# Kernel tuning notes

Hardware: AMD Instinct MI355X
Metric: run time of the kernel (lower is better)

The kernel has to match this reference:

```python
import jax, jax.numpy as jnp
import numpy as np

COMMITMENT_COST = 0.25  # pg_nn.VectorQuantizer default


def setup_inputs() -> dict:
    key = jax.random.key(0)
    k1, k2, k3, k4 = jax.random.split(key, 4)
    B, C, H, W = 32, 128, 64, 64
    D, K = 64, 512
    x = jax.random.normal(k1, (B, C, H, W), jnp.float32)
    # 1x1 conv == per-pixel linear projection; store weight as [D, C]
    conv_w = jax.random.normal(k2, (D, C), jnp.float32) * (1.0 / np.sqrt(C))
    conv_b = jax.random.normal(k3, (D,), jnp.float32) * 0.01
    # VectorQuantizer init: uniform(-1/K, 1/K)
    codebook = jax.random.uniform(k4, (K, D), jnp.float32, -1.0 / K, 1.0 / K)
    return {"x": x, "conv_w": conv_w, "conv_b": conv_b, "codebook": codebook}


def reference(x, conv_w, conv_b, codebook):
    # 1x1 conv projection: [B,C,H,W] -> [B,D,H,W]
    z = jnp.einsum('bchw,dc->bdhw', x, conv_w) + conv_b[None, :, None, None]
    B, D, H, W = z.shape
    flat = z.transpose(0, 2, 3, 1).reshape(-1, D)  # [B*H*W, D]
    # squared L2 distances to each codebook vector: [B*H*W, K]
    dists = (jnp.sum(flat * flat, axis=1, keepdims=True)
             - 2.0 * flat @ codebook.T
             + jnp.sum(codebook * codebook, axis=1))
    idx = jnp.argmin(dists, axis=1)  # [B*H*W]
    quantized = codebook[idx].reshape(B, H, W, D).transpose(0, 3, 1, 2)
    # VQ losses (commitment + embedding)
    commitment = COMMITMENT_COST * jnp.mean(jnp.square(jax.lax.stop_gradient(quantized) - z))
    emb_loss = jnp.mean(jnp.square(quantized - jax.lax.stop_gradient(z)))
    loss = commitment + emb_loss
    # straight-through estimator
    quantized_st = z + jax.lax.stop_gradient(quantized - z)
    return quantized_st, loss
```

## Files before the change

kernel.cpp:

```cpp
#include <hip/hip_runtime.h>
#include <hip/hip_bf16.h>
#include <math.h>

#define CIN   128
#define DDIM  64
#define KCB   512
#define HWSZ  4096
#define NOUTQ 8388608
#define XPAD  136

typedef short bf16x8 __attribute__((ext_vector_type(8)));
typedef float f32x4  __attribute__((ext_vector_type(4)));
typedef unsigned int u32x2 __attribute__((ext_vector_type(2)));

#define BLOB_B   84992
#define NCHUNK_B 83
#define WS_PART  86016

__device__ __forceinline__ unsigned int bcu(float f){ union{float f;unsigned int u;}v; v.f=f; return v.u; }
__device__ __forceinline__ float bcf(unsigned int u){ union{unsigned int u;float f;}v; v.u=u; return v.f; }
__device__ __forceinline__ unsigned int pkbf(float a, float b){
    union { __hip_bfloat162 h; unsigned int u; } v;
    v.h = __float22bfloat162_rn(make_float2(a, b));
    return v.u;
}

#define MFMA16(A, B, C) __builtin_amdgcn_mfma_f32_16x16x32_bf16((A), (B), (C), 0, 0, 0)

__global__ __launch_bounds__(256) void vq_prep(
    const float* __restrict__ cb, const float* __restrict__ w,
    const float* __restrict__ bias, unsigned char* __restrict__ blob)
{
    unsigned short* cbA = (unsigned short*)blob;
    unsigned short* wA  = (unsigned short*)(blob + 65536);
    float*          cbn = (float*)(blob + 81920);
    float*          bia = (float*)(blob + 83968);

    const int gid = blockIdx.x * 256 + threadIdx.x;
    {
        int k = gid >> 4, dg = gid & 15;
        f32x4 v = *(const f32x4*)(cb + (size_t)k * DDIM + dg * 4);
        u32x2 pv = { pkbf(-2.f * v[0], -2.f * v[1]), pkbf(-2.f * v[2], -2.f * v[3]) };
        int ct = k >> 4, ks = dg >> 3, lhi = (dg >> 1) & 3, ll = (k & 15) | (lhi << 4);
        *(u32x2*)(cbA + ((ct * 2 + ks) * 64 + ll) * 8 + (dg & 1) * 4) = pv;
    }
    if (gid < 2048) {
        int d = gid >> 5, cg = gid & 31;
        f32x4 v = *(const f32x4*)(w + (size_t)d * CIN + cg * 4);
        u32x2 pv = { pkbf(v[0], v[1]), pkbf(v[2], v[3]) };
        int dt = d >> 4, ks = cg >> 3, lhi = (cg >> 1) & 3, ll = (d & 15) | (lhi << 4);
        *(u32x2*)(wA + ((dt * 4 + ks) * 64 + ll) * 8 + (cg & 1) * 4) = pv;
    }
    if (gid < KCB) {
        const f32x4* row = (const f32x4*)(cb + (size_t)gid * DDIM);
        float s = 0.f;
        #pragma unroll
        for (int j = 0; j < DDIM / 4; ++j) {
            f32x4 v = row[j];
            s = fmaf(v[0], v[0], s); s = fmaf(v[1], v[1], s);
            s = fmaf(v[2], v[2], s); s = fmaf(v[3], v[3], s);
        }
        cbn[gid] = s;
    }
    if (gid < DDIM) bia[gid] = bias[gid];
}

__device__ __forceinline__ void proj_tile(
    const float (&xr)[32], unsigned short* xrow,
    const unsigned short* sWA, const float* sBias,
    int lg, int klg, int l,
    f32x4& zA, f32x4& zB, f32x4& zC, f32x4& zD, bf16x8& zb0, bf16x8& zb1)
{
    #pragma unroll
    for (int j = 0; j < 8; ++j) {
        u32x2 pv = { pkbf(xr[4*j+0], xr[4*j+1]), pkbf(xr[4*j+2], xr[4*j+3]) };
        *(u32x2*)(xrow + lg * 32 + 4 * j) = pv;
    }
    zA = *(const f32x4*)(sBias +  0 + klg);
    zB = *(const f32x4*)(sBias + 16 + klg);
    zC = *(const f32x4*)(sBias + 32 + klg);
    zD = *(const f32x4*)(sBias + 48 + klg);
    #pragma unroll
    for (int ks = 0; ks < 4; ++ks) {
        bf16x8 xf = *(const bf16x8*)(xrow + ks * 32 + lg * 8);
        bf16x8 w0 = *(const bf16x8*)(sWA + ((0 * 4 + ks) * 64 + l) * 8);
        bf16x8 w1 = *(const bf16x8*)(sWA + ((1 * 4 + ks) * 64 + l) * 8);
        bf16x8 w2 = *(const bf16x8*)(sWA + ((2 * 4 + ks) * 64 + l) * 8);
        bf16x8 w3 = *(const bf16x8*)(sWA + ((3 * 4 + ks) * 64 + l) * 8);
        zA = MFMA16(w0, xf, zA);
        zB = MFMA16(w1, xf, zB);
        zC = MFMA16(w2, xf, zC);
        zD = MFMA16(w3, xf, zD);
    }
    unsigned int* zr = (unsigned int*)xrow;
    u32x2 z0 = { pkbf(zA[0], zA[1]), pkbf(zA[2], zA[3]) };
    u32x2 z1 = { pkbf(zB[0], zB[1]), pkbf(zB[2], zB[3]) };
    u32x2 z2 = { pkbf(zC[0], zC[1]), pkbf(zC[2], zC[3]) };
    u32x2 z3 = { pkbf(zD[0], zD[1]), pkbf(zD[2], zD[3]) };
    *(u32x2*)(zr +  0 + lg * 2) = z0;
    *(u32x2*)(zr +  8 + lg * 2) = z1;
    *(u32x2*)(zr + 16 + lg * 2) = z2;
    *(u32x2*)(zr + 24 + lg * 2) = z3;
    zb0 = *(const bf16x8*)(xrow + lg * 8);
    zb1 = *(const bf16x8*)(xrow + 32 + lg * 8);
}

__global__ __launch_bounds__(1024, 4) void vq_mfma(
    const float* __restrict__ x,
    const float* __restrict__ cb,
    const unsigned char* __restrict__ blob,
    float* __restrict__ out,
    float* __restrict__ part)
{
    __shared__ __align__(16) unsigned char sFrag[BLOB_B];
    __shared__ __align__(16) unsigned short sX[16 * 16 * XPAD];
    __shared__ float sLoss[16];

    const int t   = threadIdx.x;
    const int l   = t & 63;
    const int wv  = t >> 6;
    const int p16 = l & 15;
    const int lg  = l >> 4;
    const int klg = lg * 4;

    for (int i = wv; i < NCHUNK_B; i += 16) {
        const unsigned char* g = blob + i * 1024 + l * 16;
        unsigned char* s = sFrag + i * 1024;
        __builtin_amdgcn_global_load_lds(
            (const __attribute__((address_space(1))) unsigned int*)g,
            (__attribute__((address_space(3))) unsigned int*)s, 16, 0, 0);
    }

    const int b   = blockIdx.x >> 3;
    const int hw0 = (blockIdx.x & 7) * 512 + wv * 32;
    const float* xp = x + ((size_t)b * CIN + (size_t)lg * 32) * HWSZ + hw0 + p16;
    float xr0[32], xr1[32];
    #pragma unroll
    for (int j = 0; j < 32; ++j) {
        xr0[j] = xp[(size_t)j * HWSZ];
        xr1[j] = xp[(size_t)j * HWSZ + 16];
    }
    __syncthreads();

    const unsigned short* sCbA = (const unsigned short*)sFrag;
    const unsigned short* sWA  = (const unsigned short*)(sFrag + 65536);
    const float*          sCbn = (const float*)(sFrag + 81920);
    const float*          sBias= (const float*)(sFrag + 83968);

    unsigned short* xrow = sX + wv * (16 * XPAD) + p16 * XPAD;

    f32x4 zaA0, zaA1, zaA2, zaA3, zaB0, zaB1, zaB2, zaB3;
    bf16x8 zb00, zb01, zb10, zb11;
    proj_tile(xr0, xrow, sWA, sBias, lg, klg, l, zaA0, zaA1, zaA2, zaA3, zb00, zb01);
    proj_tile(xr1, xrow, sWA, sBias, lg, klg, l, zaB0, zaB1, zaB2, zaB3, zb10, zb11);

    float rm00 = INFINITY, rm01 = INFINITY, rm10 = INFINITY, rm11 = INFINITY;
    #pragma unroll 4
    for (int ct = 0; ct < 32; ++ct) {
        f32x4 cinit = *(const f32x4*)(sCbn + ct * 16 + klg);
        bf16x8 c0 = *(const bf16x8*)(sCbA + ((ct * 2 + 0) * 64 + l) * 8);
        bf16x8 c1 = *(const bf16x8*)(sCbA + ((ct * 2 + 1) * 64 + l) * 8);
        f32x4 a0 = MFMA16(c0, zb00, cinit); a0 = MFMA16(c1, zb01, a0);
        f32x4 a1 = MFMA16(c0, zb10, cinit); a1 = MFMA16(c1, zb11, a1);
        unsigned int kb = (unsigned int)(ct * 16 + klg);
        rm00 = fminf(rm00, bcf((bcu(a0[0]) & 0xFFFFFE00u) | (kb + 0)));
        rm01 = fminf(rm01, bcf((bcu(a0[1]) & 0xFFFFFE00u) | (kb + 1)));
        rm00 = fminf(rm00, bcf((bcu(a0[2]) & 0xFFFFFE00u) | (kb + 2)));
        rm01 = fminf(rm01, bcf((bcu(a0[3]) & 0xFFFFFE00u) | (kb + 3)));
        rm10 = fminf(rm10, bcf((bcu(a1[0]) & 0xFFFFFE00u) | (kb + 0)));
        rm11 = fminf(rm11, bcf((bcu(a1[1]) & 0xFFFFFE00u) | (kb + 1)));
        rm10 = fminf(rm10, bcf((bcu(a1[2]) & 0xFFFFFE00u) | (kb + 2)));
        rm11 = fminf(rm11, bcf((bcu(a1[3]) & 0xFFFFFE00u) | (kb + 3)));
    }
    float rn0 = fminf(rm00, rm01);
    rn0 = fminf(rn0, __shfl_xor(rn0, 16, 64));
    rn0 = fminf(rn0, __shfl_xor(rn0, 32, 64));
    const int kbest0 = (int)(bcu(rn0) & 511u);
    float rn1 = fminf(rm10, rm11);
    rn1 = fminf(rn1, __shfl_xor(rn1, 16, 64));
    rn1 = fminf(rn1, __shfl_xor(rn1, 32, 64));
    const int kbest1 = (int)(bcu(rn1) & 511u);

    const float* q0r = cb + (size_t)kbest0 * DDIM;
    const float* q1r = cb + (size_t)kbest1 * DDIM;
    f32x4 qa0 = *(const f32x4*)(q0r +  0 + klg), qb0 = *(const f32x4*)(q1r +  0 + klg);
    f32x4 qa1 = *(const f32x4*)(q0r + 16 + klg), qb1 = *(const f32x4*)(q1r + 16 + klg);
    f32x4 qa2 = *(const f32x4*)(q0r + 32 + klg), qb2 = *(const f32x4*)(q1r + 32 + klg);
    f32x4 qa3 = *(const f32x4*)(q0r + 48 + klg), qb3 = *(const f32x4*)(q1r + 48 + klg);
    float lsum = 0.f;
    size_t ob = ((size_t)b * DDIM + klg) * (size_t)HWSZ + hw0 + p16;
    #pragma unroll
    for (int r = 0; r < 4; ++r) {
        float e;
        e = qa0[r] - zaA0[r]; lsum = fmaf(e, e, lsum);
        e = qb0[r] - zaB0[r]; lsum = fmaf(e, e, lsum);
        e = qa1[r] - zaA1[r]; lsum = fmaf(e, e, lsum);
        e = qb1[r] - zaB1[r]; lsum = fmaf(e, e, lsum);
        e = qa2[r] - zaA2[r]; lsum = fmaf(e, e, lsum);
        e = qb2[r] - zaB2[r]; lsum = fmaf(e, e, lsum);
        e = qa3[r] - zaA3[r]; lsum = fmaf(e, e, lsum);
        e = qb3[r] - zaB3[r]; lsum = fmaf(e, e, lsum);
        out[ob + (size_t)(r +  0) * HWSZ]      = qa0[r];
        out[ob + (size_t)(r +  0) * HWSZ + 16] = qb0[r];
        out[ob + (size_t)(r + 16) * HWSZ]      = qa1[r];
        out[ob + (size_t)(r + 16) * HWSZ + 16] = qb1[r];
        out[ob + (size_t)(r + 32) * HWSZ]      = qa2[r];
        out[ob + (size_t)(r + 32) * HWSZ + 16] = qb2[r];
        out[ob + (size_t)(r + 48) * HWSZ]      = qa3[r];
        out[ob + (size_t)(r + 48) * HWSZ + 16] = qb3[r];
    }

    #pragma unroll
    for (int off = 32; off > 0; off >>= 1)
        lsum += __shfl_down(lsum, off, 64);
    if (l == 0) sLoss[wv] = lsum;
    __syncthreads();
    if (wv == 0) {
        float v = (l < 16) ? sLoss[l] : 0.f;
        v += __shfl_down(v, 8, 64);
        v += __shfl_down(v, 4, 64);
        v += __shfl_down(v, 2, 64);
        v += __shfl_down(v, 1, 64);
        if (l == 0) part[blockIdx.x] = v;
    }
}

__global__ __launch_bounds__(256) void vq_loss(
    const float* __restrict__ part, float* __restrict__ loss_slot)
{
    __shared__ float sW[4];
    const int t = threadIdx.x;
    float s = part[t];
    #pragma unroll
    for (int off = 32; off > 0; off >>= 1) s += __shfl_down(s, off, 64);
    if ((t & 63) == 0) sW[t >> 6] = s;
    __syncthreads();
    if (t == 0)
        *loss_slot = (sW[0] + sW[1] + sW[2] + sW[3]) * (1.25f / (float)NOUTQ);
}

extern "C" void kernel_launch(void* const* d_in, const int* in_sizes, int n_in,
                              void* d_out, int out_size, void* d_ws, size_t ws_size,
                              hipStream_t stream) {
    const float* x    = (const float*)d_in[0];
    const float* w    = (const float*)d_in[1];
    const float* bias = (const float*)d_in[2];
    const float* cb   = (const float*)d_in[3];
    float* out = (float*)d_out;
    float* loss_slot = out + NOUTQ;

    unsigned char* blob = (unsigned char*)d_ws;
    float* part = (float*)(blob + WS_PART);

    vq_prep<<<32,  256,  0, stream>>>(cb, w, bias, blob);
    vq_mfma<<<256, 1024, 0, stream>>>(x, cb, blob, out, part);
    vq_loss<<<1,   256,  0, stream>>>(part, loss_slot);
}
```

Measured before the change: 42.56 us.

## Fuse loss reduction via last-block ticket and overlap x loads with LDS blob copy

Removes the separate loss-reduction kernel: each block writes its partial, increments an atomic ticket, and the last block sums all partials and writes the loss. The __syncthreads after the loads is replaced by a partial vmcnt wait plus a raw s_barrier, so the x register loads can stay in flight while the LDS blob copy completes. Launch bounds are relaxed from 4 to 2 waves per EU, which allows more registers. The partial vmcnt(48) relies on the hardware retiring memory operations in issue order, and the ticket scheme depends on a threadfence and relaxed atomic loads to be correct.

```diff
diff --git a/kernel.cpp b/kernel.cpp
--- a/kernel.cpp
+++ b/kernel.cpp
@@ -16,6 +16,7 @@
 #define BLOB_B   84992
 #define NCHUNK_B 83
 #define WS_PART  86016
+#define WS_TICK  87040
 
 __device__ __forceinline__ unsigned int bcu(float f){ union{float f;unsigned int u;}v; v.f=f; return v.u; }
 __device__ __forceinline__ float bcf(unsigned int u){ union{unsigned int u;float f;}v; v.u=u; return v.f; }
@@ -29,7 +30,8 @@
 
 __global__ __launch_bounds__(256) void vq_prep(
     const float* __restrict__ cb, const float* __restrict__ w,
-    const float* __restrict__ bias, unsigned char* __restrict__ blob)
+    const float* __restrict__ bias, unsigned char* __restrict__ blob,
+    unsigned int* __restrict__ ticket)
 {
     unsigned short* cbA = (unsigned short*)blob;
     unsigned short* wA  = (unsigned short*)(blob + 65536);
@@ -63,6 +65,7 @@
         cbn[gid] = s;
     }
     if (gid < DDIM) bia[gid] = bias[gid];
+    if (gid == 0) *ticket = 0u;
 }
 
 __device__ __forceinline__ void proj_tile(
@@ -105,12 +108,13 @@
     zb1 = *(const bf16x8*)(xrow + 32 + lg * 8);
 }
 
-__global__ __launch_bounds__(1024, 4) void vq_mfma(
+__global__ __launch_bounds__(1024, 2) void vq_mfma(
     const float* __restrict__ x,
     const float* __restrict__ cb,
     const unsigned char* __restrict__ blob,
     float* __restrict__ out,
-    float* __restrict__ part)
+    float* __restrict__ part,
+    unsigned int* __restrict__ ticket)
 {
     __shared__ __align__(16) unsigned char sFrag[BLOB_B];
     __shared__ __align__(16) unsigned short sX[16 * 16 * XPAD];
@@ -130,6 +134,7 @@
             (const __attribute__((address_space(1))) unsigned int*)g,
             (__attribute__((address_space(3))) unsigned int*)s, 16, 0, 0);
     }
+    __builtin_amdgcn_sched_barrier(0);
 
     const int b   = blockIdx.x >> 3;
     const int hw0 = (blockIdx.x & 7) * 512 + wv * 32;
@@ -140,7 +145,10 @@
         xr0[j] = xp[(size_t)j * HWSZ];
         xr1[j] = xp[(size_t)j * HWSZ + 16];
     }
-    __syncthreads();
+    __builtin_amdgcn_sched_barrier(0);
+    asm volatile("s_waitcnt vmcnt(48)" ::: "memory");
+    __builtin_amdgcn_s_barrier();
+    __builtin_amdgcn_sched_barrier(0);
 
     const unsigned short* sCbA = (const unsigned short*)sFrag;
     const unsigned short* sWA  = (const unsigned short*)(sFrag + 65536);
@@ -221,22 +229,25 @@
         v += __shfl_down(v, 4, 64);
         v += __shfl_down(v, 2, 64);
         v += __shfl_down(v, 1, 64);
-        if (l == 0) part[blockIdx.x] = v;
-    }
-}
-
-__global__ __launch_bounds__(256) void vq_loss(
-    const float* __restrict__ part, float* __restrict__ loss_slot)
-{
-    __shared__ float sW[4];
-    const int t = threadIdx.x;
-    float s = part[t];
-    #pragma unroll
-    for (int off = 32; off > 0; off >>= 1) s += __shfl_down(s, off, 64);
-    if ((t & 63) == 0) sW[t >> 6] = s;
-    __syncthreads();
-    if (t == 0)
-        *loss_slot = (sW[0] + sW[1] + sW[2] + sW[3]) * (1.25f / (float)NOUTQ);
+        unsigned int old = 0u;
+        if (l == 0) {
+            part[blockIdx.x] = v;
+            __threadfence();
+            old = atomicAdd(ticket, 1u);
+        }
+        old = __shfl((int)old, 0, 64);
+        if (old == 255u) {
+            float s = 0.f;
+            #pragma unroll
+            for (int j = 0; j < 4; ++j)
+                s += __hip_atomic_load(&part[l + j * 64],
+                                       __ATOMIC_RELAXED, __HIP_MEMORY_SCOPE_AGENT);
+            #pragma unroll
+            for (int off = 32; off > 0; off >>= 1)
+                s += __shfl_down(s, off, 64);
+            if (l == 0) out[NOUTQ] = s * (1.25f / (float)NOUTQ);
+        }
+    }
 }
 
 extern "C" void kernel_launch(void* const* d_in, const int* in_sizes, int n_in,
@@ -247,12 +258,11 @@
     const float* bias = (const float*)d_in[2];
     const float* cb   = (const float*)d_in[3];
     float* out = (float*)d_out;
-    float* loss_slot = out + NOUTQ;
 
     unsigned char* blob = (unsigned char*)d_ws;
     float* part = (float*)(blob + WS_PART);
-
-    vq_prep<<<32,  256,  0, stream>>>(cb, w, bias, blob);
-    vq_mfma<<<256, 1024, 0, stream>>>(x, cb, blob, out, part);
-    vq_loss<<<1,   256,  0, stream>>>(part, loss_slot);
-}
+    unsigned int* tick = (unsigned int*)(blob + WS_TICK);
+
+    vq_prep<<<32,  256,  0, stream>>>(cb, w, bias, blob, tick);
+    vq_mfma<<<256, 1024, 0, stream>>>(x, cb, blob, out, part, tick);
+}
```

Result: slower. 51.53 us (+21.1%).

## Load x straight into bf16 MFMA fragments and derive loss from min distances

Applied to the files above, without the earlier changes.

Each lane now reads and packs x directly into bf16 MFMA operand fragments, so the per-wave LDS staging of x and its round trip are gone and the LDS buffer shrinks to a z-only tile. The VQ loss is now computed algebraically as the selected minimum distance plus ||z||^2, which removes the per-element (q - z)^2 work. The quantized output is written with a new mapping where each lane stores 32 channels for one pixel, making stores coalesced across pixels. The risk is loss precision: the minimum distance comes from bf16 MFMA with index bits packed into the mantissa.

```diff
diff --git a/kernel.cpp b/kernel.cpp
--- a/kernel.cpp
+++ b/kernel.cpp
@@ -7,7 +7,7 @@
 #define KCB   512
 #define HWSZ  4096
 #define NOUTQ 8388608
-#define XPAD  136
+#define ZPAD  72
 
 typedef short bf16x8 __attribute__((ext_vector_type(8)));
 typedef float f32x4  __attribute__((ext_vector_type(4)));
@@ -65,34 +65,45 @@
     if (gid < DDIM) bia[gid] = bias[gid];
 }
 
-__device__ __forceinline__ void proj_tile(
-    const float (&xr)[32], unsigned short* xrow,
-    const unsigned short* sWA, const float* sBias,
+#define LOADXF(xq, lgv, F0, F1, F2, F3)                                     \
+    {                                                                       \
+        union { unsigned int u[4]; bf16x8 v; } c0_, c1_, c2_, c3_;          \
+        _Pragma("unroll")                                                   \
+        for (int p = 0; p < 4; ++p) {                                       \
+            const float* a0 = (xq) + (size_t)(  0 + (lgv)*8 + 2*p) * HWSZ;  \
+            const float* a1 = (xq) + (size_t)( 32 + (lgv)*8 + 2*p) * HWSZ;  \
+            const float* a2 = (xq) + (size_t)( 64 + (lgv)*8 + 2*p) * HWSZ;  \
+            const float* a3 = (xq) + (size_t)( 96 + (lgv)*8 + 2*p) * HWSZ;  \
+            c0_.u[p] = pkbf(a0[0], a0[HWSZ]);                               \
+            c1_.u[p] = pkbf(a1[0], a1[HWSZ]);                               \
+            c2_.u[p] = pkbf(a2[0], a2[HWSZ]);                               \
+            c3_.u[p] = pkbf(a3[0], a3[HWSZ]);                               \
+        }                                                                   \
+        F0 = c0_.v; F1 = c1_.v; F2 = c2_.v; F3 = c3_.v;                     \
+    }
+
+__device__ __forceinline__ void proj_mfma(
+    bf16x8 f0, bf16x8 f1, bf16x8 f2, bf16x8 f3,
+    unsigned short* zrow, const unsigned short* sWA, const float* sBias,
     int lg, int klg, int l,
     f32x4& zA, f32x4& zB, f32x4& zC, f32x4& zD, bf16x8& zb0, bf16x8& zb1)
 {
-    #pragma unroll
-    for (int j = 0; j < 8; ++j) {
-        u32x2 pv = { pkbf(xr[4*j+0], xr[4*j+1]), pkbf(xr[4*j+2], xr[4*j+3]) };
-        *(u32x2*)(xrow + lg * 32 + 4 * j) = pv;
-    }
     zA = *(const f32x4*)(sBias +  0 + klg);
     zB = *(const f32x4*)(sBias + 16 + klg);
     zC = *(const f32x4*)(sBias + 32 + klg);
     zD = *(const f32x4*)(sBias + 48 + klg);
-    #pragma unroll
-    for (int ks = 0; ks < 4; ++ks) {
-        bf16x8 xf = *(const bf16x8*)(xrow + ks * 32 + lg * 8);
-        bf16x8 w0 = *(const bf16x8*)(sWA + ((0 * 4 + ks) * 64 + l) * 8);
-        bf16x8 w1 = *(const bf16x8*)(sWA + ((1 * 4 + ks) * 64 + l) * 8);
-        bf16x8 w2 = *(const bf16x8*)(sWA + ((2 * 4 + ks) * 64 + l) * 8);
-        bf16x8 w3 = *(const bf16x8*)(sWA + ((3 * 4 + ks) * 64 + l) * 8);
-        zA = MFMA16(w0, xf, zA);
-        zB = MFMA16(w1, xf, zB);
-        zC = MFMA16(w2, xf, zC);
-        zD = MFMA16(w3, xf, zD);
-    }
-    unsigned int* zr = (unsigned int*)xrow;
+    #define PSTEP(ks, xf) {                                             \
+        bf16x8 w0 = *(const bf16x8*)(sWA + ((0 * 4 + ks) * 64 + l) * 8);\
+        bf16x8 w1 = *(const bf16x8*)(sWA + ((1 * 4 + ks) * 64 + l) * 8);\
+        bf16x8 w2 = *(const bf16x8*)(sWA + ((2 * 4 + ks) * 64 + l) * 8);\
+        bf16x8 w3 = *(const bf16x8*)(sWA + ((3 * 4 + ks) * 64 + l) * 8);\
+        zA = MFMA16(w0, xf, zA);                                        \
+        zB = MFMA16(w1, xf, zB);                                        \
+        zC = MFMA16(w2, xf, zC);                                        \
+        zD = MFMA16(w3, xf, zD); }
+    PSTEP(0, f0) PSTEP(1, f1) PSTEP(2, f2) PSTEP(3, f3)
+    #undef PSTEP
+    unsigned int* zr = (unsigned int*)zrow;
     u32x2 z0 = { pkbf(zA[0], zA[1]), pkbf(zA[2], zA[3]) };
     u32x2 z1 = { pkbf(zB[0], zB[1]), pkbf(zB[2], zB[3]) };
     u32x2 z2 = { pkbf(zC[0], zC[1]), pkbf(zC[2], zC[3]) };
@@ -101,8 +112,8 @@
     *(u32x2*)(zr +  8 + lg * 2) = z1;
     *(u32x2*)(zr + 16 + lg * 2) = z2;
     *(u32x2*)(zr + 24 + lg * 2) = z3;
-    zb0 = *(const bf16x8*)(xrow + lg * 8);
-    zb1 = *(const bf16x8*)(xrow + 32 + lg * 8);
+    zb0 = *(const bf16x8*)(zrow + lg * 8);
+    zb1 = *(const bf16x8*)(zrow + 32 + lg * 8);
 }
 
 __global__ __launch_bounds__(1024, 4) void vq_mfma(
@@ -113,7 +124,7 @@
     float* __restrict__ part)
 {
     __shared__ __align__(16) unsigned char sFrag[BLOB_B];
-    __shared__ __align__(16) unsigned short sX[16 * 16 * XPAD];
+    __shared__ __align__(16) unsigned short sZ[16 * 16 * ZPAD];
     __shared__ float sLoss[16];
 
     const int t   = threadIdx.x;
@@ -133,26 +144,24 @@
 
     const int b   = blockIdx.x >> 3;
     const int hw0 = (blockIdx.x & 7) * 512 + wv * 32;
-    const float* xp = x + ((size_t)b * CIN + (size_t)lg * 32) * HWSZ + hw0 + p16;
-    float xr0[32], xr1[32];
-    #pragma unroll
-    for (int j = 0; j < 32; ++j) {
-        xr0[j] = xp[(size_t)j * HWSZ];
-        xr1[j] = xp[(size_t)j * HWSZ + 16];
-    }
+    const float* xq = x + (size_t)b * CIN * HWSZ + hw0 + p16;
+    bf16x8 xa0, xa1, xa2, xa3, xb0, xb1, xb2, xb3;
+    LOADXF(xq,      lg, xa0, xa1, xa2, xa3)
+    LOADXF(xq + 16, lg, xb0, xb1, xb2, xb3)
     __syncthreads();
 
     const unsigned short* sCbA = (const unsigned short*)sFrag;
     const unsigned short* sWA  = (const unsigned short*)(sFrag + 65536);
     const float*          sCbn = (const float*)(sFrag + 81920);
     const float*          sBias= (const float*)(sFrag + 83968);
-
-    unsigned short* xrow = sX + wv * (16 * XPAD) + p16 * XPAD;
+    unsigned short* zrow = sZ + wv * (16 * ZPAD) + p16 * ZPAD;
 
     f32x4 zaA0, zaA1, zaA2, zaA3, zaB0, zaB1, zaB2, zaB3;
     bf16x8 zb00, zb01, zb10, zb11;
-    proj_tile(xr0, xrow, sWA, sBias, lg, klg, l, zaA0, zaA1, zaA2, zaA3, zb00, zb01);
-    proj_tile(xr1, xrow, sWA, sBias, lg, klg, l, zaB0, zaB1, zaB2, zaB3, zb10, zb11);
+    proj_mfma(xa0, xa1, xa2, xa3, zrow, sWA, sBias, lg, klg, l,
+              zaA0, zaA1, zaA2, zaA3, zb00, zb01);
+    proj_mfma(xb0, xb1, xb2, xb3, zrow, sWA, sBias, lg, klg, l,
+              zaB0, zaB1, zaB2, zaB3, zb10, zb11);
 
     float rm00 = INFINITY, rm01 = INFINITY, rm10 = INFINITY, rm11 = INFINITY;
     #pragma unroll 4
@@ -181,39 +190,40 @@
     rn1 = fminf(rn1, __shfl_xor(rn1, 32, 64));
     const int kbest1 = (int)(bcu(rn1) & 511u);
 
-    const float* q0r = cb + (size_t)kbest0 * DDIM;
-    const float* q1r = cb + (size_t)kbest1 * DDIM;
-    f32x4 qa0 = *(const f32x4*)(q0r +  0 + klg), qb0 = *(const f32x4*)(q1r +  0 + klg);
-    f32x4 qa1 = *(const f32x4*)(q0r + 16 + klg), qb1 = *(const f32x4*)(q1r + 16 + klg);
-    f32x4 qa2 = *(const f32x4*)(q0r + 32 + klg), qb2 = *(const f32x4*)(q1r + 32 + klg);
-    f32x4 qa3 = *(const f32x4*)(q0r + 48 + klg), qb3 = *(const f32x4*)(q1r + 48 + klg);
-    float lsum = 0.f;
-    size_t ob = ((size_t)b * DDIM + klg) * (size_t)HWSZ + hw0 + p16;
+    float zn0 = 0.f, zn1 = 0.f;
     #pragma unroll
     for (int r = 0; r < 4; ++r) {
-        float e;
-        e = qa0[r] - zaA0[r]; lsum = fmaf(e, e, lsum);
-        e = qb0[r] - zaB0[r]; lsum = fmaf(e, e, lsum);
-        e = qa1[r] - zaA1[r]; lsum = fmaf(e, e, lsum);
-        e = qb1[r] - zaB1[r]; lsum = fmaf(e, e, lsum);
-        e = qa2[r] - zaA2[r]; lsum = fmaf(e, e, lsum);
-        e = qb2[r] - zaB2[r]; lsum = fmaf(e, e, lsum);
-        e = qa3[r] - zaA3[r]; lsum = fmaf(e, e, lsum);
-        e = qb3[r] - zaB3[r]; lsum = fmaf(e, e, lsum);
-        out[ob + (size_t)(r +  0) * HWSZ]      = qa0[r];
-        out[ob + (size_t)(r +  0) * HWSZ + 16] = qb0[r];
-        out[ob + (size_t)(r + 16) * HWSZ]      = qa1[r];
-        out[ob + (size_t)(r + 16) * HWSZ + 16] = qb1[r];
-        out[ob + (size_t)(r + 32) * HWSZ]      = qa2[r];
-        out[ob + (size_t)(r + 32) * HWSZ + 16] = qb2[r];
-        out[ob + (size_t)(r + 48) * HWSZ]      = qa3[r];
-        out[ob + (size_t)(r + 48) * HWSZ + 16] = qb3[r];
-    }
-
+        zn0 = fmaf(zaA0[r], zaA0[r], zn0); zn0 = fmaf(zaA1[r], zaA1[r], zn0);
+        zn0 = fmaf(zaA2[r], zaA2[r], zn0); zn0 = fmaf(zaA3[r], zaA3[r], zn0);
+        zn1 = fmaf(zaB0[r], zaB0[r], zn1); zn1 = fmaf(zaB1[r], zaB1[r], zn1);
+        zn1 = fmaf(zaB2[r], zaB2[r], zn1); zn1 = fmaf(zaB3[r], zaB3[r], zn1);
+    }
+    zn0 += __shfl_xor(zn0, 16, 64); zn0 += __shfl_xor(zn0, 32, 64);
+    zn1 += __shfl_xor(zn1, 16, 64); zn1 += __shfl_xor(zn1, 32, 64);
+
+    {
+        const int px = l & 31;
+        const int dh = (l >> 5) * 32;
+        const int kbs = (px & 16) ? kbest1 : kbest0;
+        const f32x4* qv = (const f32x4*)(cb + (size_t)kbs * DDIM + dh);
+        f32x4 q0 = qv[0], q1 = qv[1], q2 = qv[2], q3 = qv[3];
+        f32x4 q4 = qv[4], q5 = qv[5], q6 = qv[6], q7 = qv[7];
+        size_t base = ((size_t)b * DDIM + dh) * (size_t)HWSZ + hw0 + px;
+        #define QST(i, qq) \
+            out[base + (size_t)(4*(i)+0) * HWSZ] = qq[0]; \
+            out[base + (size_t)(4*(i)+1) * HWSZ] = qq[1]; \
+            out[base + (size_t)(4*(i)+2) * HWSZ] = qq[2]; \
+            out[base + (size_t)(4*(i)+3) * HWSZ] = qq[3];
+        QST(0, q0) QST(1, q1) QST(2, q2) QST(3, q3)
+        QST(4, q4) QST(5, q5) QST(6, q6) QST(7, q7)
+        #undef QST
+    }
+
+    float lv = 0.25f * ((rn0 + zn0) + (rn1 + zn1));
     #pragma unroll
     for (int off = 32; off > 0; off >>= 1)
-        lsum += __shfl_down(lsum, off, 64);
-    if (l == 0) sLoss[wv] = lsum;
+        lv += __shfl_down(lv, off, 64);
+    if (l == 0) sLoss[wv] = lv;
     __syncthreads();
     if (wv == 0) {
         float v = (l < 16) ? sLoss[l] : 0.f;
```

After: 47.97 us. +12.7%, slower.
